# Kernel optimization log

Hardware: AMD Instinct MI355X
Metric: run time of the kernel (lower is better)

The kernel has to match this reference:

```python
import jax, jax.numpy as jnp
from jax import lax
import numpy as np
import math

# --- static config (matches init_kwargs) ---
B, L, C_IN = 64, 1024, 16
D, H, D_FF = 256, 8, 1024
HS, E_LAYERS, OUT = 256, 2, 1
MA, FACTOR = 25, 3
TOP_K = int(FACTOR * math.log(L))  # 20


def _ln(x, g, b, eps=1e-5):
    m = x.mean(-1, keepdims=True)
    v = ((x - m) ** 2).mean(-1, keepdims=True)
    return (x - m) / jnp.sqrt(v + eps) * g + b


def _series_decomp(x, k):
    # x: [B, L, C]; replicate-pad then moving average (AvgPool1d stride 1)
    pad = (k - 1) // 2
    front = jnp.repeat(x[:, :1, :], pad, axis=1)
    end = jnp.repeat(x[:, -1:, :], pad, axis=1)
    xp = jnp.concatenate([front, x, end], axis=1)  # [B, L+k-1, C]
    cs = jnp.cumsum(xp, axis=1)
    cs = jnp.concatenate([jnp.zeros_like(cs[:, :1]), cs], axis=1)
    mm = (cs[:, k:] - cs[:, :-k]) / k  # [B, L, C]
    return x - mm, mm


def _autocorrelation(q, k, v):
    # q,k,v: [B, L, H, E] -> eval-mode Autoformer AutoCorrelation
    Bq, Lq, Hq, Eq = q.shape
    qf = jnp.fft.rfft(q.transpose(0, 2, 3, 1), axis=-1)  # [B,H,E,F]
    kf = jnp.fft.rfft(k.transpose(0, 2, 3, 1), axis=-1)
    corr = jnp.fft.irfft(qf * jnp.conj(kf), n=Lq, axis=-1)  # [B,H,E,L]
    mean_value = corr.mean(axis=(1, 2))  # [B, L]
    weights, delay = lax.top_k(mean_value, TOP_K)  # [B, K]
    tmp_corr = jax.nn.softmax(weights, axis=-1)
    vals = v.transpose(0, 2, 3, 1)  # [B,H,E,L]
    init = jnp.arange(Lq)

    def step(acc, dw):
        d, w = dw  # d: [B] int, w: [B] float
        idx = (init[None, :] + d[:, None]) % Lq  # circular delayed gather == roll
        pat = jnp.take_along_axis(vals, idx[:, None, None, :], axis=-1)
        return acc + pat * w[:, None, None, None], None

    agg, _ = lax.scan(step, jnp.zeros_like(vals), (delay.T, tmp_corr.T))
    return agg.transpose(0, 3, 1, 2)  # [B, L, H, E]


def _forward(x_enc, conv1_w, conv1_b, conv2_w, conv2_b, cnn_ln_g, cnn_ln_b,
             proj_w, proj_b, proj_ln_g, proj_ln_b,
             Wq, bq, Wk, bk, Wv, bv, Wo, bo, Wff1, Wff2,
             rp1_w, rp1_b, rp_ln_g, rp_ln_b, rp2_w, rp2_b):
    Bb = x_enc.shape[0]
    dn = ('NCH', 'OIH', 'NCH')
    # CNN frontend (dropout = identity in eval)
    h = lax.conv_general_dilated(x_enc.transpose(0, 2, 1), conv1_w, (1,), [(1, 1)],
                                 dimension_numbers=dn) + conv1_b[None, :, None]
    h = jax.nn.relu(h)
    h = lax.conv_general_dilated(h, conv2_w, (1,), [(1, 1)],
                                 dimension_numbers=dn) + conv2_b[None, :, None]
    h = jax.nn.relu(h)
    enc = _ln(h.transpose(0, 2, 1), cnn_ln_g, cnn_ln_b)  # [B, L, D]

    pooled_parts = []
    for i in range(E_LAYERS):
        q = (enc @ Wq[i] + bq[i]).reshape(Bb, L, H, D // H)
        k = (enc @ Wk[i] + bk[i]).reshape(Bb, L, H, D // H)
        v = (enc @ Wv[i] + bv[i]).reshape(Bb, L, H, D // H)
        ac = _autocorrelation(q, k, v).reshape(Bb, L, D)
        new_x = ac @ Wo[i] + bo[i]
        x = enc + new_x
        x, _ = _series_decomp(x, MA)
        y = jax.nn.gelu(jnp.einsum('bld,fd->blf', x, Wff1[i]), approximate=False)
        y = jnp.einsum('blf,df->bld', y, Wff2[i])
        enc, _ = _series_decomp(x + y, MA)
        pooled_parts.append(enc[:, -1, :])

    pooled = jnp.concatenate(pooled_parts, axis=-1)  # [B, e_layers*D]
    input_embed = _ln(jax.nn.relu(x_enc.reshape(Bb, -1) @ proj_w + proj_b),
                      proj_ln_g, proj_ln_b)  # [B, HS]
    final = jnp.concatenate([pooled, input_embed], axis=-1)
    o = jax.nn.relu(final @ rp1_w + rp1_b)
    o = _ln(o, rp_ln_g, rp_ln_b)
    o = o @ rp2_w + rp2_b  # [B, 1]
    return o.squeeze(-1)


def setup_inputs() -> dict:
    key = jax.random.key(0)
    ks = iter(jax.random.split(key, 32))

    def nrm(shape, s=0.02):
        return jax.random.normal(next(ks), shape, jnp.float32) * s

    inp = {
        'x_enc': jax.random.normal(next(ks), (B, L, C_IN), jnp.float32),
        'conv1_w': nrm((D, C_IN, 3), 0.1), 'conv1_b': jnp.zeros((D,), jnp.float32),
        'conv2_w': nrm((D, D, 3), 0.05), 'conv2_b': jnp.zeros((D,), jnp.float32),
        'cnn_ln_g': jnp.ones((D,), jnp.float32), 'cnn_ln_b': jnp.zeros((D,), jnp.float32),
        'proj_w': nrm((L * C_IN, HS)), 'proj_b': jnp.zeros((HS,), jnp.float32),
        'proj_ln_g': jnp.ones((HS,), jnp.float32), 'proj_ln_b': jnp.zeros((HS,), jnp.float32),
        'Wq': nrm((E_LAYERS, D, D)), 'bq': jnp.zeros((E_LAYERS, D), jnp.float32),
        'Wk': nrm((E_LAYERS, D, D)), 'bk': jnp.zeros((E_LAYERS, D), jnp.float32),
        'Wv': nrm((E_LAYERS, D, D)), 'bv': jnp.zeros((E_LAYERS, D), jnp.float32),
        'Wo': nrm((E_LAYERS, D, D)), 'bo': jnp.zeros((E_LAYERS, D), jnp.float32),
        'Wff1': nrm((E_LAYERS, D_FF, D)),
        'Wff2': nrm((E_LAYERS, D, D_FF)),
        'rp1_w': nrm((E_LAYERS * D + HS, HS)), 'rp1_b': jnp.zeros((HS,), jnp.float32),
        'rp_ln_g': jnp.ones((HS,), jnp.float32), 'rp_ln_b': jnp.zeros((HS,), jnp.float32),
        'rp2_w': nrm((HS, OUT)), 'rp2_b': jnp.zeros((OUT,), jnp.float32),
    }
    return inp


def reference(x_enc, conv1_w, conv1_b, conv2_w, conv2_b, cnn_ln_g, cnn_ln_b,
              proj_w, proj_b, proj_ln_g, proj_ln_b,
              Wq, bq, Wk, bk, Wv, bv, Wo, bo, Wff1, Wff2,
              rp1_w, rp1_b, rp_ln_g, rp_ln_b, rp2_w, rp2_b):
    return _forward(x_enc, conv1_w, conv1_b, conv2_w, conv2_b, cnn_ln_g, cnn_ln_b,
                    proj_w, proj_b, proj_ln_g, proj_ln_b,
                    Wq, bq, Wk, bk, Wv, bv, Wo, bo, Wff1, Wff2,
                    rp1_w, rp1_b, rp_ln_g, rp_ln_b, rp2_w, rp2_b)
```

## Files before the change

kernel.cpp:

```cpp
#include <hip/hip_runtime.h>
#include <math.h>

#define FLAG_ACC     1
#define FLAG_RELU    2
#define FLAG_GELU    4
#define FLAG_ABF16   8
#define FLAG_OBF16  16
#define FLAG_RESB16 32

typedef __attribute__((ext_vector_type(8))) short short8;
typedef __attribute__((ext_vector_type(4))) short short4v;
typedef __attribute__((ext_vector_type(4))) float f32x4;

__device__ __forceinline__ short f2bf(float f) {
  unsigned u = __builtin_bit_cast(unsigned, f);
  unsigned r = u + 0x7fffu + ((u >> 16) & 1u);
  return (short)(r >> 16);
}
__device__ __forceinline__ float bf2f(short s) {
  unsigned u = ((unsigned)(unsigned short)s) << 16;
  return __builtin_bit_cast(float, u);
}
__device__ __forceinline__ void load_lds16(const void* g, void* lds) {
  __builtin_amdgcn_global_load_lds(
      (const __attribute__((address_space(1))) void*)g,
      (__attribute__((address_space(3))) void*)lds, 16, 0, 0);
}

__global__ __launch_bounds__(256) void gemm_f32(
    const float* __restrict__ A, const float* __restrict__ B, float* __restrict__ C,
    int M, int N, int K, int a_shift,
    const float* __restrict__ bias, const float* __restrict__ residual, int flags)
{
  __shared__ float As[16][65];
  __shared__ float Bs[16][64];
  const int tid = threadIdx.x;
  const int tx = tid & 15, ty = tid >> 4;
  const int row0 = blockIdx.y * 64;
  const int col0 = blockIdx.x * 64;
  int kbeg = 0, kend = K;
  if ((int)gridDim.z > 1) {
    int kchunk = ((K + (int)gridDim.z - 1) / (int)gridDim.z + 15) & ~15;
    kbeg = (int)blockIdx.z * kchunk;
    kend = min(K, kbeg + kchunk);
  }
  float acc[4][4] = {};
  const int a_m = tid >> 2;
  const int a_k = (tid & 3) << 2;
  const int b_n = (tid & 15) << 2;
  const int b_k = tid >> 4;
  for (int k0 = kbeg; k0 < kend; k0 += 16) {
    int srow = row0 + a_m + a_shift;
    float4 av = make_float4(0.f, 0.f, 0.f, 0.f);
    if (srow >= 0 && srow < M)
      av = *reinterpret_cast<const float4*>(A + (long long)srow * K + (k0 + a_k));
    As[a_k + 0][a_m] = av.x; As[a_k + 1][a_m] = av.y;
    As[a_k + 2][a_m] = av.z; As[a_k + 3][a_m] = av.w;
    float4 bv = make_float4(0.f, 0.f, 0.f, 0.f);
    int brow = k0 + b_k;
    if (brow < K)
      bv = *reinterpret_cast<const float4*>(B + (long long)brow * N + (col0 + b_n));
    Bs[b_k][b_n + 0] = bv.x; Bs[b_k][b_n + 1] = bv.y;
    Bs[b_k][b_n + 2] = bv.z; Bs[b_k][b_n + 3] = bv.w;
    __syncthreads();
#pragma unroll
    for (int kk = 0; kk < 16; kk++) {
      float ar[4], br[4];
#pragma unroll
      for (int i = 0; i < 4; i++) ar[i] = As[kk][ty * 4 + i];
#pragma unroll
      for (int j = 0; j < 4; j++) br[j] = Bs[kk][tx * 4 + j];
#pragma unroll
      for (int i = 0; i < 4; i++)
#pragma unroll
        for (int j = 0; j < 4; j++)
          acc[i][j] += ar[i] * br[j];
    }
    __syncthreads();
  }
  if ((int)gridDim.z > 1) {
#pragma unroll
    for (int i = 0; i < 4; i++) {
      int r = row0 + ty * 4 + i; if (r >= M) continue;
#pragma unroll
      for (int j = 0; j < 4; j++) {
        int c = col0 + tx * 4 + j; if (c >= N) continue;
        atomicAdd(&C[(long long)r * N + c], acc[i][j]);
      }
    }
    return;
  }
#pragma unroll
  for (int i = 0; i < 4; i++) {
    int r = row0 + ty * 4 + i; if (r >= M) continue;
#pragma unroll
    for (int j = 0; j < 4; j++) {
      int c = col0 + tx * 4 + j; if (c >= N) continue;
      float v = acc[i][j];
      if (bias)     v += bias[c];
      if (residual) v += residual[(long long)r * N + c];
      if (flags & FLAG_ACC)  v += C[(long long)r * N + c];
      if (flags & FLAG_RELU) v = fmaxf(v, 0.f);
      if (flags & FLAG_GELU) v = 0.5f * v * (1.f + erff(v * 0.70710678118654752f));
      C[(long long)r * N + c] = v;
    }
  }
}

__global__ __launch_bounds__(256) void gemm_bf16_bt(
    const void* __restrict__ Av, const short* __restrict__ Btb, void* __restrict__ Cv,
    const float* __restrict__ residual, const float* __restrict__ bias,
    int M, int N, int K, int lda, int flags, int tapped)
{
  __shared__ __align__(16) short Asl[8192];
  __shared__ __align__(16) short Bsl[8192];
  const int tid = threadIdx.x;
  const int row0 = blockIdx.x * 128;
  const int col0 = blockIdx.y * 128;
  const int lane = tid & 63;
  const int wave = tid >> 6;
  const int wm = (wave >> 1) * 64;
  const int wn = (wave & 1) * 64;
  const int fm = lane & 15;
  const int k8c = lane >> 4;
  const int mr = tid >> 1;
  const int mkc = (tid & 1) * 4;
  const int msw = mr & 7;
  const bool a_dma = (flags & FLAG_ABF16) && !tapped;

  f32x4 acc[4][4] = {};
  for (int k0 = 0; k0 < K; k0 += 64) {
    __syncthreads();
#pragma unroll
    for (int u = 0; u < 4; u++) {
      int p = (wave * 4 + u) * 64 + lane;
      int r = p >> 3;
      int kc = (p & 7) ^ (r & 7);
      load_lds16(Btb + (long long)(col0 + r) * K + k0 + kc * 8,
                 (char*)Bsl + (wave * 4 + u) * 1024);
    }
    if (a_dma) {
      const short* Ab = (const short*)Av;
#pragma unroll
      for (int u = 0; u < 4; u++) {
        int p = (wave * 4 + u) * 64 + lane;
        int r = p >> 3;
        int kc = (p & 7) ^ (r & 7);
        load_lds16(Ab + (long long)(row0 + r) * lda + k0 + kc * 8,
                   (char*)Asl + (wave * 4 + u) * 1024);
      }
    } else {
      int arow = row0 + mr + (tapped ? (k0 >> 8) - 1 : 0);
      int acol = tapped ? (k0 & 255) : k0;
      bool ok = (arow >= 0 && arow < M);
      if (flags & FLAG_ABF16) {
        const short* ga = (const short*)Av + (long long)arow * lda + acol + mkc * 8;
        short8 z;
#pragma unroll
        for (int u = 0; u < 8; u++) z[u] = 0;
#pragma unroll
        for (int j = 0; j < 4; j++) {
          short8 v = ok ? *(const short8*)(ga + j * 8) : z;
          *(short8*)&Asl[(mr * 8 + ((mkc + j) ^ msw)) * 8] = v;
        }
      } else {
        const float* ga = (const float*)Av + (long long)arow * lda + acol + mkc * 8;
#pragma unroll
        for (int j = 0; j < 4; j++) {
          float4 f0 = make_float4(0.f,0.f,0.f,0.f), f1 = f0;
          if (ok) { f0 = *(const float4*)(ga + j * 8); f1 = *(const float4*)(ga + j * 8 + 4); }
          short8 v;
          v[0]=f2bf(f0.x); v[1]=f2bf(f0.y); v[2]=f2bf(f0.z); v[3]=f2bf(f0.w);
          v[4]=f2bf(f1.x); v[5]=f2bf(f1.y); v[6]=f2bf(f1.z); v[7]=f2bf(f1.w);
          *(short8*)&Asl[(mr * 8 + ((mkc + j) ^ msw)) * 8] = v;
        }
      }
    }
    __syncthreads();
#pragma unroll
    for (int kk8 = 0; kk8 < 8; kk8 += 4) {
      short8 af[4], bf[4];
#pragma unroll
      for (int i = 0; i < 4; i++) {
        int r = wm + i * 16 + fm;
        af[i] = *(short8*)&Asl[(r * 8 + ((kk8 + k8c) ^ (r & 7))) * 8];
      }
#pragma unroll
      for (int j = 0; j < 4; j++) {
        int r = wn + j * 16 + fm;
        bf[j] = *(short8*)&Bsl[(r * 8 + ((kk8 + k8c) ^ (r & 7))) * 8];
      }
#pragma unroll
      for (int i = 0; i < 4; i++)
#pragma unroll
        for (int j = 0; j < 4; j++)
          acc[i][j] = __builtin_amdgcn_mfma_f32_16x16x32_bf16(af[i], bf[j], acc[i][j], 0, 0, 0);
    }
  }
#pragma unroll
  for (int i = 0; i < 4; i++) {
    const int mbase = row0 + wm + i * 16 + (lane >> 4) * 4;
#pragma unroll
    for (int j = 0; j < 4; j++) {
      const int n = col0 + wn + j * 16 + fm;
      const float bs = bias ? bias[n] : 0.f;
#pragma unroll
      for (int r = 0; r < 4; r++) {
        long long idx = (long long)(mbase + r) * N + n;
        float v = acc[i][j][r] + bs;
        if (residual) {
          if (flags & FLAG_RESB16) v += bf2f(((const short*)residual)[idx]);
          else                     v += residual[idx];
        }
        if (flags & FLAG_ACC)  v += ((const float*)Cv)[idx];
        if (flags & FLAG_RELU) v = fmaxf(v, 0.f);
        if (flags & FLAG_GELU) v = 0.5f * v * (1.f + erff(v * 0.70710678118654752f));
        if (flags & FLAG_OBF16) ((short*)Cv)[idx] = f2bf(v);
        else                    ((float*)Cv)[idx] = v;
      }
    }
  }
}

__global__ __launch_bounds__(256) void gemm_qkT(
    const short* __restrict__ Ab, const short* __restrict__ Bth,
    const short* __restrict__ Btl, float* __restrict__ QT,
    const float* __restrict__ bias, int K)
{
  __shared__ __align__(16) char smem[24576];
  short* Asl = (short*)smem;
  short* Bhi = (short*)(smem + 8192);
  short* Blo = (short*)(smem + 16384);
  const int tid = threadIdx.x;
  const int row0 = blockIdx.x * 128;
  const int col0 = blockIdx.y * 128;
  const int lane = tid & 63;
  const int wave = tid >> 6;
  const int wm = (wave >> 1) * 64;
  const int wn = (wave & 1) * 64;
  const int fm = lane & 15;
  const int k8c = lane >> 4;

  f32x4 acc[4][4] = {};
  for (int k0 = 0; k0 < K; k0 += 32) {
    __syncthreads();
#pragma unroll
    for (int u = 0; u < 2; u++) {
      int p = (wave + u * 4) * 64 + lane;
      int r = p >> 2;
      int kc = (p & 3) ^ ((r >> 1) & 3);
      long long ao = (long long)(row0 + r) * 256 + k0 + kc * 8;
      long long go = (long long)(col0 + r) * K + k0 + kc * 8;
      int lo = (wave + u * 4) * 1024;
      load_lds16(Ab + ao, (char*)Asl + lo);
      load_lds16(Bth + go, (char*)Bhi + lo);
      load_lds16(Btl + go, (char*)Blo + lo);
    }
    __syncthreads();
    short8 af[4], bh[4], bl[4];
#pragma unroll
    for (int i = 0; i < 4; i++) {
      int r = wm + i * 16 + fm;
      af[i] = *(short8*)&Asl[(r * 4 + (k8c ^ ((r >> 1) & 3))) * 8];
    }
#pragma unroll
    for (int j = 0; j < 4; j++) {
      int r = wn + j * 16 + fm;
      int p = (r * 4 + (k8c ^ ((r >> 1) & 3))) * 8;
      bh[j] = *(short8*)&Bhi[p];
      bl[j] = *(short8*)&Blo[p];
    }
#pragma unroll
    for (int i = 0; i < 4; i++)
#pragma unroll
      for (int j = 0; j < 4; j++) {
        acc[i][j] = __builtin_amdgcn_mfma_f32_16x16x32_bf16(af[i], bh[j], acc[i][j], 0, 0, 0);
        acc[i][j] = __builtin_amdgcn_mfma_f32_16x16x32_bf16(af[i], bl[j], acc[i][j], 0, 0, 0);
      }
  }
#pragma unroll
  for (int i = 0; i < 4; i++) {
    const int mbase = row0 + wm + i * 16 + (lane >> 4) * 4;
    const int bb = mbase >> 10;
    const int l  = mbase & 1023;
#pragma unroll
    for (int j = 0; j < 4; j++) {
      const int n = col0 + wn + j * 16 + fm;
      const float bs = bias[n];
      float4 o = make_float4(acc[i][j][0] + bs, acc[i][j][1] + bs,
                             acc[i][j][2] + bs, acc[i][j][3] + bs);
      *(float4*)&QT[((long long)(bb * 512 + n) << 10) + l] = o;
    }
  }
}

#define SKW(i) ((i) + ((i) >> 5))

__device__ __forceinline__ int rev4_10(int f) {
  return ((f & 3) << 8) | (((f >> 2) & 3) << 6) | (((f >> 4) & 3) << 4)
       | (((f >> 6) & 3) << 2) | ((f >> 8) & 3);
}

template<int M, bool INV>
__device__ __forceinline__ void fft_stage(const float2* __restrict__ s,
                                          float2* __restrict__ d,
                                          const float2* __restrict__ tw, int t) {
  constexpr int LOG2M = (M == 256) ? 8 : (M == 64) ? 6 : (M == 16) ? 4 : (M == 4) ? 2 : 0;
  const int j = t & (M - 1);
  const int base = ((t >> LOG2M) << (LOG2M + 2)) | j;
  float2 a = s[SKW(base)];
  float2 b = s[SKW(base + M)];
  float2 c = s[SKW(base + 2 * M)];
  float2 e = s[SKW(base + 3 * M)];
  float t0r = a.x + c.x, t0i = a.y + c.y;
  float t1r = a.x - c.x, t1i = a.y - c.y;
  float t2r = b.x + e.x, t2i = b.y + e.y;
  float t3r = b.x - e.x, t3i = b.y - e.y;
  float y0r = t0r + t2r, y0i = t0i + t2i;
  float y2r = t0r - t2r, y2i = t0i - t2i;
  float y1r, y1i, y3r, y3i;
  if (!INV) { y1r = t1r + t3i; y1i = t1i - t3r; y3r = t1r - t3i; y3i = t1i + t3r; }
  else      { y1r = t1r - t3i; y1i = t1i + t3r; y3r = t1r + t3i; y3i = t1i - t3r; }
  float2 w = tw[SKW(j << (8 - LOG2M))];
  float c1 = w.x, s1 = INV ? -w.y : w.y;
  float c2 = c1 * c1 - s1 * s1, s2 = 2.f * c1 * s1;
  float c3 = c2 * c1 - s2 * s1, s3 = c2 * s1 + s2 * c1;
  d[SKW(base)]         = make_float2(y0r, y0i);
  d[SKW(base + M)]     = make_float2(y1r * c1 - y1i * s1, y1r * s1 + y1i * c1);
  d[SKW(base + 2 * M)] = make_float2(y2r * c2 - y2i * s2, y2r * s2 + y2i * c2);
  d[SKW(base + 3 * M)] = make_float2(y3r * c3 - y3i * s3, y3r * s3 + y3i * c3);
}

__global__ __launch_bounds__(256) void fft_cross(
    const float* __restrict__ QT, float* __restrict__ Rpart)
{
  __shared__ float2 ping[1056], pong[1056], tw[264];
  const int tid = threadIdx.x;
  const int b = blockIdx.x & 63;
  const int g = blockIdx.x >> 6;
  {
    float s, c;
    sincosf(-1.5707963267948966f * (float)tid * (1.f / 256.f), &s, &c);
    tw[SKW(tid)] = make_float2(c, s);
  }
  const float* Qb = QT + (long long)b * 524288;
  const int c0 = g * 32;
  float4 qv = *(const float4*)(Qb + ((long long)c0 << 10) + tid * 4);
  float4 kv = *(const float4*)(Qb + ((long long)(256 + c0) << 10) + tid * 4);
  float aR[4] = {0.f, 0.f, 0.f, 0.f}, aI[4] = {0.f, 0.f, 0.f, 0.f};
  __syncthreads();
  for (int cc = 0; cc < 32; cc++) {
    const int i0 = tid * 4;
    ping[SKW(i0 + 0)] = make_float2(qv.x, kv.x);
    ping[SKW(i0 + 1)] = make_float2(qv.y, kv.y);
    ping[SKW(i0 + 2)] = make_float2(qv.z, kv.z);
    ping[SKW(i0 + 3)] = make_float2(qv.w, kv.w);
    if (cc < 31) {
      int c = c0 + cc + 1;
      qv = *(const float4*)(Qb + ((long long)c << 10) + tid * 4);
      kv = *(const float4*)(Qb + ((long long)(256 + c) << 10) + tid * 4);
    }
    __syncthreads();
    fft_stage<256, false>(ping, pong, tw, tid); __syncthreads();
    fft_stage<64,  false>(pong, ping, tw, tid); __syncthreads();
    fft_stage<16,  false>(ping, pong, tw, tid); __syncthreads();
    fft_stage<4,   false>(pong, ping, tw, tid); __syncthreads();
    fft_stage<1,   false>(ping, pong, tw, tid); __syncthreads();
#pragma unroll
    for (int u = 0; u < 4; u++) {
      int f = tid + (u << 8);
      float2 z1 = pong[SKW(rev4_10(f))];
      float2 z2 = pong[SKW(rev4_10((1024 - f) & 1023))];
      float Qr = 0.5f * (z1.x + z2.x), Qi = 0.5f * (z1.y - z2.y);
      float Kr = 0.5f * (z1.y + z2.y), Ki = 0.5f * (z2.x - z1.x);
      aR[u] += Qr * Kr + Qi * Ki;
      aI[u] += Qi * Kr - Qr * Ki;
    }
  }
  float* Rp = Rpart + (long long)(g * 64 + b) * 2048;
#pragma unroll
  for (int u = 0; u < 4; u++) {
    Rp[tid + (u << 8)] = aR[u];
    Rp[1024 + tid + (u << 8)] = aI[u];
  }
}

__global__ __launch_bounds__(256) void fft_inv(
    const float* __restrict__ Rpart, float* __restrict__ MV)
{
  __shared__ float2 ping[1056], pong[1056], tw[264];
  const int tid = threadIdx.x;
  const int b = blockIdx.x;
  {
    float s, c;
    sincosf(-1.5707963267948966f * (float)tid * (1.f / 256.f), &s, &c);
    tw[SKW(tid)] = make_float2(c, s);
  }
#pragma unroll
  for (int u = 0; u < 4; u++) {
    int f = tid + (u << 8);
    float sr = 0.f, si = 0.f;
#pragma unroll
    for (int g = 0; g < 8; g++) {
      const float* Rp = Rpart + (long long)(g * 64 + b) * 2048;
      sr += Rp[f];
      si += Rp[1024 + f];
    }
    ping[SKW(f)] = make_float2(sr, si);
  }
  __syncthreads();
  fft_stage<256, true>(ping, pong, tw, tid); __syncthreads();
  fft_stage<64,  true>(pong, ping, tw, tid); __syncthreads();
  fft_stage<16,  true>(ping, pong, tw, tid); __syncthreads();
  fft_stage<4,   true>(pong, ping, tw, tid); __syncthreads();
  fft_stage<1,   true>(ping, pong, tw, tid); __syncthreads();
  const float sc = 1.f / (1024.f * 256.f);
#pragma unroll
  for (int u = 0; u < 4; u++) {
    int p = tid + (u << 8);
    MV[(long long)b * 1024 + rev4_10(p)] = pong[SKW(p)].x * sc;
  }
}

__global__ void prep_weights(
    const float* __restrict__ conv2_w, const float* __restrict__ Wq,
    const float* __restrict__ Wk, const float* __restrict__ Wff1,
    const float* __restrict__ Wff2,
    const float* __restrict__ bq, const float* __restrict__ bk,
    short* __restrict__ CB2Tb, short* __restrict__ QKTH, short* __restrict__ QKTL,
    short* __restrict__ WFF1b, short* __restrict__ WFF2b, float* __restrict__ BQK)
{
  const int total = 196608 + 262144 + 524288 + 524288 + 1024;
  for (int idx = blockIdx.x * 256 + threadIdx.x; idx < total;
       idx += gridDim.x * 256) {
    int t = idx;
    if (t < 196608) {
      int o = t / 768, rem = t % 768, kk = rem >> 8, i = rem & 255;
      CB2Tb[t] = f2bf(conv2_w[(o * 256 + i) * 3 + kk]);
    } else if ((t -= 196608) < 262144) {
      int L = t >> 17, rem = t & 131071, r = rem >> 8, k = rem & 255;
      float val = (r < 256) ? Wq[L * 65536 + k * 256 + r]
                            : Wk[L * 65536 + k * 256 + (r - 256)];
      short h = f2bf(val);
      QKTH[t] = h;
      QKTL[t] = f2bf(val - bf2f(h));
    } else if ((t -= 262144) < 524288) {
      WFF1b[t] = f2bf(Wff1[t]);
    } else if ((t -= 524288) < 524288) {
      WFF2b[t] = f2bf(Wff2[t]);
    } else {
      t -= 524288;
      int L = t >> 9, j = t & 511;
      BQK[t] = (j < 256) ? bq[L * 256 + j] : bk[L * 256 + (j - 256)];
    }
  }
}

__global__ void vo_finish(const float* __restrict__ WVO, const float* __restrict__ Wo,
                          const float* __restrict__ bv, const float* __restrict__ bo,
                          short* __restrict__ WVOTb, float* __restrict__ BVO)
{
  const int total = 131072 + 512;
  for (int idx = blockIdx.x * 256 + threadIdx.x; idx < total;
       idx += gridDim.x * 256) {
    if (idx < 131072) {
      int L = idx >> 16, rem = idx & 65535, n = rem >> 8, k = rem & 255;
      WVOTb[idx] = f2bf(WVO[L * 65536 + k * 256 + n]);
    } else {
      int j = idx - 131072;
      int L = j >> 8, n = j & 255;
      float acc = bo[L * 256 + n];
      for (int k = 0; k < 256; k++)
        acc += bv[L * 256 + k] * Wo[(long long)L * 65536 + k * 256 + n];
      BVO[j] = acc;
    }
  }
}

__global__ __launch_bounds__(256) void conv1_direct(
    const float* __restrict__ x, const float* __restrict__ w,
    const float* __restrict__ bias, short* __restrict__ out)
{
  __shared__ float xs[66][16];
  const int b = blockIdx.y, lg = blockIdx.x, tid = threadIdx.x;
  const int l0 = lg * 64;
  for (int idx = tid; idx < 1056; idx += 256) {
    int r = idx >> 4, c = idx & 15;
    int l = l0 + r - 1;
    xs[r][c] = (l >= 0 && l < 1024) ? x[((long long)b * 1024 + l) * 16 + c] : 0.f;
  }
  float wr[48];
#pragma unroll
  for (int u = 0; u < 48; u++) wr[u] = w[tid * 48 + u];
  const float bs = bias[tid];
  __syncthreads();
  for (int r = 0; r < 64; r++) {
    float acc = bs;
#pragma unroll
    for (int i = 0; i < 16; i++) {
      acc += xs[r + 0][i] * wr[i * 3 + 0];
      acc += xs[r + 1][i] * wr[i * 3 + 1];
      acc += xs[r + 2][i] * wr[i * 3 + 2];
    }
    out[((long long)b * 1024 + l0 + r) * 256 + tid] = f2bf(fmaxf(acc, 0.f));
  }
}

__global__ void fixup_conv_b(short* __restrict__ h, const short* __restrict__ src,
                             const float* __restrict__ w, const float* __restrict__ bias)
{
  int b = blockIdx.x >> 1;
  int l = (blockIdx.x & 1) ? 1023 : 0;
  int o = threadIdx.x;
  float acc = bias[o];
  for (int kk = 0; kk < 3; kk++) {
    int t = l + kk - 1;
    if (t < 0 || t > 1023) continue;
    const short* srow = src + ((long long)b * 1024 + t) * 256;
    const float* wrow = w + (long long)o * 256 * 3 + kk;
    for (int i = 0; i < 256; i++) acc += bf2f(srow[i]) * wrow[(long long)i * 3];
  }
  h[((long long)b * 1024 + l) * 256 + o] = f2bf(fmaxf(acc, 0.f));
}

__global__ __launch_bounds__(256) void ln_rows4(
    const float* __restrict__ in, float* __restrict__ out,
    const float* __restrict__ g, const float* __restrict__ b,
    int prerelu, int out_stride, int out_off)
{
  const int row = blockIdx.x * 4 + (threadIdx.x >> 6);
  const int lane = threadIdx.x & 63;
  float4 x = ((const float4*)(in + (long long)row * 256))[lane];
  if (prerelu) {
    x.x = fmaxf(x.x, 0.f); x.y = fmaxf(x.y, 0.f);
    x.z = fmaxf(x.z, 0.f); x.w = fmaxf(x.w, 0.f);
  }
  float s = x.x + x.y + x.z + x.w;
#pragma unroll
  for (int o = 32; o > 0; o >>= 1) s += __shfl_xor(s, o, 64);
  float mean = s * (1.f / 256.f);
  float4 d = make_float4(x.x - mean, x.y - mean, x.z - mean, x.w - mean);
  float s2 = d.x * d.x + d.y * d.y + d.z * d.z + d.w * d.w;
#pragma unroll
  for (int o = 32; o > 0; o >>= 1) s2 += __shfl_xor(s2, o, 64);
  float rsd = rsqrtf(s2 * (1.f / 256.f) + 1e-5f);
  float4 gg = ((const float4*)g)[lane];
  float4 bb = ((const float4*)b)[lane];
  float4 o4 = make_float4(d.x * rsd * gg.x + bb.x, d.y * rsd * gg.y + bb.y,
                          d.z * rsd * gg.z + bb.z, d.w * rsd * gg.w + bb.w);
  ((float4*)(out + (long long)row * out_stride + out_off))[lane] = o4;
}

__global__ __launch_bounds__(256) void ln_rows4bb(
    const short* __restrict__ in, short* __restrict__ out,
    const float* __restrict__ g, const float* __restrict__ b)
{
  const int row = blockIdx.x * 4 + (threadIdx.x >> 6);
  const int lane = threadIdx.x & 63;
  short4v xb = ((const short4v*)in)[(long long)row * 64 + lane];
  float4 x = make_float4(bf2f(xb[0]), bf2f(xb[1]), bf2f(xb[2]), bf2f(xb[3]));
  float s = x.x + x.y + x.z + x.w;
#pragma unroll
  for (int o = 32; o > 0; o >>= 1) s += __shfl_xor(s, o, 64);
  float mean = s * (1.f / 256.f);
  float4 d = make_float4(x.x - mean, x.y - mean, x.z - mean, x.w - mean);
  float s2 = d.x * d.x + d.y * d.y + d.z * d.z + d.w * d.w;
#pragma unroll
  for (int o = 32; o > 0; o >>= 1) s2 += __shfl_xor(s2, o, 64);
  float rsd = rsqrtf(s2 * (1.f / 256.f) + 1e-5f);
  float4 gg = ((const float4*)g)[lane];
  float4 bb = ((const float4*)b)[lane];
  short4v o4;
  o4[0] = f2bf(d.x * rsd * gg.x + bb.x);
  o4[1] = f2bf(d.y * rsd * gg.y + bb.y);
  o4[2] = f2bf(d.z * rsd * gg.z + bb.z);
  o4[3] = f2bf(d.w * rsd * gg.w + bb.w);
  ((short4v*)out)[(long long)row * 64 + lane] = o4;
}

__global__ void decomp4bf(const short* __restrict__ in, short* __restrict__ out,
                          float* __restrict__ fin, int finoff)
{
  const int id = blockIdx.x;
  const int c = id & 7;
  const int s = id >> 3;
  const int b = c + 8 * (s >> 8);
  const int lg = s & 255;
  const int l = lg * 4 + (threadIdx.x >> 6);
  const int c4 = threadIdx.x & 63;
  const short4v* base = (const short4v*)(in + (long long)b * 262144);
  float4 acc = make_float4(0.f, 0.f, 0.f, 0.f);
#pragma unroll
  for (int j = -12; j <= 12; j++) {
    int t = l + j;
    t = t < 0 ? 0 : (t > 1023 ? 1023 : t);
    short4v x = base[t * 64 + c4];
    acc.x += bf2f(x[0]); acc.y += bf2f(x[1]);
    acc.z += bf2f(x[2]); acc.w += bf2f(x[3]);
  }
  short4v x0 = base[l * 64 + c4];
  float4 o = make_float4(bf2f(x0[0]) - acc.x * (1.f / 25.f),
                         bf2f(x0[1]) - acc.y * (1.f / 25.f),
                         bf2f(x0[2]) - acc.z * (1.f / 25.f),
                         bf2f(x0[3]) - acc.w * (1.f / 25.f));
  short4v ob;
  ob[0] = f2bf(o.x); ob[1] = f2bf(o.y); ob[2] = f2bf(o.z); ob[3] = f2bf(o.w);
  ((short4v*)out)[((long long)b * 1024 + l) * 64 + c4] = ob;
  if (l == 1023) {
    float* f = fin + (long long)b * 768 + finoff + c4 * 4;
    f[0] = o.x; f[1] = o.y; f[2] = o.z; f[3] = o.w;
  }
}

__global__ void decomp4b(const short* __restrict__ in, short* __restrict__ out)
{
  const int id = blockIdx.x;
  const int c = id & 7;
  const int s = id >> 3;
  const int b = c + 8 * (s >> 8);
  const int lg = s & 255;
  const int l = lg * 4 + (threadIdx.x >> 6);
  const int c4 = threadIdx.x & 63;
  const short4v* base = (const short4v*)(in + (long long)b * 262144);
  float4 acc = make_float4(0.f, 0.f, 0.f, 0.f);
#pragma unroll
  for (int j = -12; j <= 12; j++) {
    int t = l + j;
    t = t < 0 ? 0 : (t > 1023 ? 1023 : t);
    short4v x = base[t * 64 + c4];
    acc.x += bf2f(x[0]); acc.y += bf2f(x[1]);
    acc.z += bf2f(x[2]); acc.w += bf2f(x[3]);
  }
  short4v x0 = base[l * 64 + c4];
  short4v o;
  o[0] = f2bf(bf2f(x0[0]) - acc.x * (1.f / 25.f));
  o[1] = f2bf(bf2f(x0[1]) - acc.y * (1.f / 25.f));
  o[2] = f2bf(bf2f(x0[2]) - acc.z * (1.f / 25.f));
  o[3] = f2bf(bf2f(x0[3]) - acc.w * (1.f / 25.f));
  ((short4v*)(out + (long long)b * 262144))[l * 64 + c4] = o;
}

__global__ __launch_bounds__(64) void topk_softmax_wave(
    const float* __restrict__ mv, float* __restrict__ wts, int* __restrict__ dly)
{
  const int b = blockIdx.x, lane = threadIdx.x;
  float v[16];
#pragma unroll
  for (int j = 0; j < 16; j++)
    v[j] = mv[(long long)b * 1024 + lane + 64 * j];
  float selv = 0.f; int seli = 0;
  for (int it = 0; it < 20; it++) {
    float bv = -1e30f; int bi = 0x7fffffff;
#pragma unroll
    for (int j = 0; j < 16; j++) {
      float x = v[j]; int idx = lane + 64 * j;
      if (x > bv || (x == bv && idx < bi)) { bv = x; bi = idx; }
    }
#pragma unroll
    for (int off = 32; off > 0; off >>= 1) {
      float ov = __shfl_xor(bv, off, 64);
      int   oi = __shfl_xor(bi, off, 64);
      if (ov > bv || (ov == bv && oi < bi)) { bv = ov; bi = oi; }
    }
    if (lane == it) { selv = bv; seli = bi; }
    if ((bi & 63) == lane) v[bi >> 6] = -1e30f;
  }
  const float w0 = __shfl(selv, 0, 64);
  float e = (lane < 20) ? __expf(selv - w0) : 0.f;
  float s = e;
#pragma unroll
  for (int off = 32; off > 0; off >>= 1) s += __shfl_xor(s, off, 64);
  if (lane < 20) {
    wts[b * 20 + lane] = e / s;
    dly[b * 20 + lane] = seli;
  }
}

__global__ void agg4b(const short* __restrict__ enc, const float* __restrict__ wts,
                      const int* __restrict__ dly, short* __restrict__ out)
{
  const int id = blockIdx.x;
  const int c = id & 7;
  const int s = id >> 3;
  const int b = c + 8 * (s >> 8);
  const int lg = s & 255;
  const int l = lg * 4 + (threadIdx.x >> 6);
  const int c4 = threadIdx.x & 63;
  const short4v* vb = (const short4v*)(enc + (long long)b * 262144);
  float4 acc = make_float4(0.f, 0.f, 0.f, 0.f);
  for (int kk = 0; kk < 20; kk++) {
    int d = dly[b * 20 + kk];
    float w = wts[b * 20 + kk];
    short4v x = vb[((l + d) & 1023) * 64 + c4];
    acc.x += w * bf2f(x[0]); acc.y += w * bf2f(x[1]);
    acc.z += w * bf2f(x[2]); acc.w += w * bf2f(x[3]);
  }
  short4v o;
  o[0] = f2bf(acc.x); o[1] = f2bf(acc.y); o[2] = f2bf(acc.z); o[3] = f2bf(acc.w);
  ((short4v*)(out + (long long)b * 262144))[l * 64 + c4] = o;
}

__global__ void init_bias(float* __restrict__ C, const float* __restrict__ bias)
{
  C[(long long)blockIdx.x * 256 + threadIdx.x] = bias[threadIdx.x];
}

__global__ void rp2_kernel(const float* __restrict__ x, const float* __restrict__ w,
                           const float* __restrict__ bias, float* __restrict__ out)
{
  __shared__ float red[4];
  int b = blockIdx.x, tid = threadIdx.x;
  float p = x[b * 256 + tid] * w[tid];
#pragma unroll
  for (int o = 32; o > 0; o >>= 1) p += __shfl_down(p, o, 64);
  if ((tid & 63) == 0) red[tid >> 6] = p;
  __syncthreads();
  if (tid == 0) out[b] = red[0] + red[1] + red[2] + red[3] + bias[0];
}

static inline void gemm(hipStream_t s, const float* A, const float* B, float* C,
                        int M, int N, int K, int shift, const float* bias,
                        const float* res, int flags, int splitz = 1)
{
  dim3 g((N + 63) / 64, (M + 63) / 64, splitz);
  gemm_f32<<<g, dim3(256), 0, s>>>(A, B, C, M, N, K, shift, bias, res, flags);
}

extern "C" void kernel_launch(void* const* d_in, const int* in_sizes, int n_in,
                              void* d_out, int out_size, void* d_ws, size_t ws_size,
                              hipStream_t stream)
{
  const float* x_enc  = (const float*)d_in[0];
  const float* conv1_w= (const float*)d_in[1];
  const float* conv1_b= (const float*)d_in[2];
  const float* conv2_w= (const float*)d_in[3];
  const float* conv2_b= (const float*)d_in[4];
  const float* cnn_g  = (const float*)d_in[5];
  const float* cnn_b  = (const float*)d_in[6];
  const float* proj_w = (const float*)d_in[7];
  const float* proj_b = (const float*)d_in[8];
  const float* pln_g  = (const float*)d_in[9];
  const float* pln_b  = (const float*)d_in[10];
  const float* Wq     = (const float*)d_in[11];
  const float* bq     = (const float*)d_in[12];
  const float* Wk     = (const float*)d_in[13];
  const float* bk     = (const float*)d_in[14];
  const float* Wv     = (const float*)d_in[15];
  const float* bv     = (const float*)d_in[16];
  const float* Wo     = (const float*)d_in[17];
  const float* bo     = (const float*)d_in[18];
  const float* Wff1   = (const float*)d_in[19];
  const float* Wff2   = (const float*)d_in[20];
  const float* rp1_w  = (const float*)d_in[21];
  const float* rp1_b  = (const float*)d_in[22];
  const float* rln_g  = (const float*)d_in[23];
  const float* rln_b  = (const float*)d_in[24];
  const float* rp2_w  = (const float*)d_in[25];
  const float* rp2_b  = (const float*)d_in[26];
  (void)in_sizes; (void)n_in;

  const size_t BLD = 64ull * 1024 * 256;
  size_t need;
  {
    size_t o = 3 * BLD
             + 98304 + 131072 + 131072 + 262144 + 262144
             + 65536 + 512 + 1024
             + 1048576 + 1280 + 1280 + 16384 + 49152 + 16384 + 16384;
    need = o * sizeof(float);
  }
  if (ws_size < need) {
    hipMemsetAsync(d_out, 0, (size_t)out_size * sizeof(float), stream);
    return;
  }

  float* ws = (float*)d_ws;
  size_t off = 0;
  auto alloc = [&](size_t n) { float* p = ws + off; off += n; return p; };
  float* BUF0 = alloc(BLD);
  float* BUF1 = alloc(BLD);
  float* BUF2 = alloc(BLD);
  short* CB2Tb = (short*)alloc(98304);
  short* QKTH  = (short*)alloc(131072);
  short* QKTL  = (short*)alloc(131072);
  short* WFF1b = (short*)alloc(262144);
  short* WFF2b = (short*)alloc(262144);
  short* WVOTb = (short*)alloc(65536);
  float* BVO  = alloc(512);
  float* BQK  = alloc(1024);
  float* MV16 = alloc(1048576);
  float* WTS  = alloc(1280);
  int*   DLY  = (int*)alloc(1280);
  float* PE   = alloc(16384);
  float* FIN  = alloc(49152);
  float* O1   = alloc(16384);
  float* O2   = alloc(16384);
  float* WVO  = BUF0;
  short* ENC  = (short*)BUF2;
  float* QT   = BUF0;
  float* MV   = BUF2 + 8388608;

  const int M = 65536;
  dim3 blk(256);

  prep_weights<<<1024, blk, 0, stream>>>(conv2_w, Wq, Wk, Wff1, Wff2, bq, bk,
                                         CB2Tb, QKTH, QKTL, WFF1b, WFF2b, BQK);
  for (int i = 0; i < 2; i++)
    gemm(stream, Wv + (size_t)i * 65536, Wo + (size_t)i * 65536,
         WVO + (size_t)i * 65536, 256, 256, 256, 0, nullptr, nullptr, 0);
  vo_finish<<<516, blk, 0, stream>>>(WVO, Wo, bv, bo, WVOTb, BVO);

  conv1_direct<<<dim3(16, 64), blk, 0, stream>>>(x_enc, conv1_w, conv1_b, (short*)BUF0);
  gemm_bf16_bt<<<dim3(512, 2), blk, 0, stream>>>(
      BUF0, CB2Tb, BUF1, nullptr, conv2_b, M, 256, 768, 256,
      FLAG_ABF16 | FLAG_RELU | FLAG_OBF16, 1);
  fixup_conv_b<<<128, blk, 0, stream>>>((short*)BUF1, (const short*)BUF0,
                                        conv2_w, conv2_b);
  ln_rows4bb<<<16384, blk, 0, stream>>>((const short*)BUF1, ENC, cnn_g, cnn_b);

  for (int i = 0; i < 2; i++) {
    gemm_qkT<<<dim3(512, 4), blk, 0, stream>>>(
        ENC, QKTH + (size_t)i * 131072, QKTL + (size_t)i * 131072,
        QT, BQK + i * 512, 256);
    fft_cross<<<512, blk, 0, stream>>>(QT, MV16);
    fft_inv<<<64, blk, 0, stream>>>(MV16, MV);
    topk_softmax_wave<<<64, dim3(64), 0, stream>>>(MV, WTS, DLY);
    agg4b<<<dim3(16384), blk, 0, stream>>>(ENC, WTS, DLY, (short*)BUF0);
    gemm_bf16_bt<<<dim3(512, 2), blk, 0, stream>>>(
        BUF0, WVOTb + (size_t)i * 65536, BUF1, (const float*)ENC, BVO + i * 256,
        M, 256, 256, 256, FLAG_ABF16 | FLAG_OBF16 | FLAG_RESB16, 0);
    decomp4b<<<16384, blk, 0, stream>>>((const short*)BUF1, (short*)BUF0);
    for (int c = 0; c < 2; c++) {
      const short* xd = (const short*)BUF0 + (size_t)c * 32768 * 256;
      gemm_bf16_bt<<<dim3(256, 8), blk, 0, stream>>>(
          xd, WFF1b + (size_t)i * 262144, BUF2, nullptr, nullptr,
          32768, 1024, 256, 256, FLAG_ABF16 | FLAG_GELU | FLAG_OBF16, 0);
      gemm_bf16_bt<<<dim3(256, 2), blk, 0, stream>>>(
          BUF2, WFF2b + (size_t)i * 262144,
          (short*)BUF1 + (size_t)c * 32768 * 256,
          (const float*)xd, nullptr,
          32768, 256, 1024, 1024, FLAG_ABF16 | FLAG_RESB16 | FLAG_OBF16, 0);
    }
    decomp4bf<<<16384, blk, 0, stream>>>((const short*)BUF1, ENC, FIN, i * 256);
  }

  init_bias<<<64, blk, 0, stream>>>(PE, proj_b);
  gemm(stream, x_enc, proj_w, PE, 64, 256, 16384, 0, nullptr, nullptr, 0, 32);
  ln_rows4<<<16, blk, 0, stream>>>(PE, FIN, pln_g, pln_b, 1, 768, 512);
  init_bias<<<64, blk, 0, stream>>>(O1, rp1_b);
  gemm(stream, FIN, rp1_w, O1, 64, 256, 768, 0, nullptr, nullptr, 0, 4);
  ln_rows4<<<16, blk, 0, stream>>>(O1, O2, rln_g, rln_b, 1, 256, 0);
  rp2_kernel<<<64, blk, 0, stream>>>(O2, rp2_w, rp2_b, (float*)d_out);
}
```

Baseline: 1.494 ms.

## Batch four channel FFTs per block in place and double the fft_cross grid

The FFT stage is rewritten to run in place and to process four channel pairs per thread per stage, so the twiddle load and barriers are amortized across four transforms. fft_cross now launches 1024 blocks of 16 channels each instead of 512 blocks of 32, which gives more parallelism. fft_inv reduces 16 partial spectra instead of 8, and the partial and MV buffers are reassigned. The cost is about 34KB of LDS per block for the four buffers, which may lower occupancy, plus more partial-sum traffic in fft_inv.

```diff
diff --git a/kernel.cpp b/kernel.cpp
--- a/kernel.cpp
+++ b/kernel.cpp
@@ -301,40 +301,44 @@
        | (((f >> 6) & 3) << 2) | ((f >> 8) & 3);
 }
 
-template<int M, bool INV>
-__device__ __forceinline__ void fft_stage(const float2* __restrict__ s,
-                                          float2* __restrict__ d,
-                                          const float2* __restrict__ tw, int t) {
+template<int M, bool INV, int NCH>
+__device__ __forceinline__ void fft_stageN(float2 (*__restrict__ buf)[1056],
+                                           const float2* __restrict__ tw, int t) {
   constexpr int LOG2M = (M == 256) ? 8 : (M == 64) ? 6 : (M == 16) ? 4 : (M == 4) ? 2 : 0;
   const int j = t & (M - 1);
   const int base = ((t >> LOG2M) << (LOG2M + 2)) | j;
-  float2 a = s[SKW(base)];
-  float2 b = s[SKW(base + M)];
-  float2 c = s[SKW(base + 2 * M)];
-  float2 e = s[SKW(base + 3 * M)];
-  float t0r = a.x + c.x, t0i = a.y + c.y;
-  float t1r = a.x - c.x, t1i = a.y - c.y;
-  float t2r = b.x + e.x, t2i = b.y + e.y;
-  float t3r = b.x - e.x, t3i = b.y - e.y;
-  float y0r = t0r + t2r, y0i = t0i + t2i;
-  float y2r = t0r - t2r, y2i = t0i - t2i;
-  float y1r, y1i, y3r, y3i;
-  if (!INV) { y1r = t1r + t3i; y1i = t1i - t3r; y3r = t1r - t3i; y3i = t1i + t3r; }
-  else      { y1r = t1r - t3i; y1i = t1i + t3r; y3r = t1r + t3i; y3i = t1i - t3r; }
   float2 w = tw[SKW(j << (8 - LOG2M))];
-  float c1 = w.x, s1 = INV ? -w.y : w.y;
-  float c2 = c1 * c1 - s1 * s1, s2 = 2.f * c1 * s1;
-  float c3 = c2 * c1 - s2 * s1, s3 = c2 * s1 + s2 * c1;
-  d[SKW(base)]         = make_float2(y0r, y0i);
-  d[SKW(base + M)]     = make_float2(y1r * c1 - y1i * s1, y1r * s1 + y1i * c1);
-  d[SKW(base + 2 * M)] = make_float2(y2r * c2 - y2i * s2, y2r * s2 + y2i * c2);
-  d[SKW(base + 3 * M)] = make_float2(y3r * c3 - y3i * s3, y3r * s3 + y3i * c3);
+  const float c1 = w.x, s1 = INV ? -w.y : w.y;
+  const float c2 = c1 * c1 - s1 * s1, s2 = 2.f * c1 * s1;
+  const float c3 = c2 * c1 - s2 * s1, s3 = c2 * s1 + s2 * c1;
+#pragma unroll
+  for (int ch = 0; ch < NCH; ch++) {
+    float2* s = buf[ch];
+    float2 a0 = s[SKW(base)];
+    float2 b0 = s[SKW(base + M)];
+    float2 d0 = s[SKW(base + 2 * M)];
+    float2 e0 = s[SKW(base + 3 * M)];
+    float t0r = a0.x + d0.x, t0i = a0.y + d0.y;
+    float t1r = a0.x - d0.x, t1i = a0.y - d0.y;
+    float t2r = b0.x + e0.x, t2i = b0.y + e0.y;
+    float t3r = b0.x - e0.x, t3i = b0.y - e0.y;
+    float y0r = t0r + t2r, y0i = t0i + t2i;
+    float y2r = t0r - t2r, y2i = t0i - t2i;
+    float y1r, y1i, y3r, y3i;
+    if (!INV) { y1r = t1r + t3i; y1i = t1i - t3r; y3r = t1r - t3i; y3i = t1i + t3r; }
+    else      { y1r = t1r - t3i; y1i = t1i + t3r; y3r = t1r + t3i; y3i = t1i - t3r; }
+    s[SKW(base)]         = make_float2(y0r, y0i);
+    s[SKW(base + M)]     = make_float2(y1r * c1 - y1i * s1, y1r * s1 + y1i * c1);
+    s[SKW(base + 2 * M)] = make_float2(y2r * c2 - y2i * s2, y2r * s2 + y2i * c2);
+    s[SKW(base + 3 * M)] = make_float2(y3r * c3 - y3i * s3, y3r * s3 + y3i * c3);
+  }
 }
 
 __global__ __launch_bounds__(256) void fft_cross(
     const float* __restrict__ QT, float* __restrict__ Rpart)
 {
-  __shared__ float2 ping[1056], pong[1056], tw[264];
+  __shared__ float2 buf[4][1056];
+  __shared__ float2 tw[264];
   const int tid = threadIdx.x;
   const int b = blockIdx.x & 63;
   const int g = blockIdx.x >> 6;
@@ -344,38 +348,54 @@
     tw[SKW(tid)] = make_float2(c, s);
   }
   const float* Qb = QT + (long long)b * 524288;
-  const int c0 = g * 32;
-  float4 qv = *(const float4*)(Qb + ((long long)c0 << 10) + tid * 4);
-  float4 kv = *(const float4*)(Qb + ((long long)(256 + c0) << 10) + tid * 4);
+  const int c0 = g * 16;
+  float4 qv[4], kv[4];
+#pragma unroll
+  for (int c = 0; c < 4; c++) {
+    qv[c] = *(const float4*)(Qb + ((long long)(c0 + c) << 10) + tid * 4);
+    kv[c] = *(const float4*)(Qb + ((long long)(256 + c0 + c) << 10) + tid * 4);
+  }
   float aR[4] = {0.f, 0.f, 0.f, 0.f}, aI[4] = {0.f, 0.f, 0.f, 0.f};
   __syncthreads();
-  for (int cc = 0; cc < 32; cc++) {
+  for (int q4 = 0; q4 < 4; q4++) {
     const int i0 = tid * 4;
-    ping[SKW(i0 + 0)] = make_float2(qv.x, kv.x);
-    ping[SKW(i0 + 1)] = make_float2(qv.y, kv.y);
-    ping[SKW(i0 + 2)] = make_float2(qv.z, kv.z);
-    ping[SKW(i0 + 3)] = make_float2(qv.w, kv.w);
-    if (cc < 31) {
-      int c = c0 + cc + 1;
-      qv = *(const float4*)(Qb + ((long long)c << 10) + tid * 4);
-      kv = *(const float4*)(Qb + ((long long)(256 + c) << 10) + tid * 4);
+#pragma unroll
+    for (int c = 0; c < 4; c++) {
+      buf[c][SKW(i0 + 0)] = make_float2(qv[c].x, kv[c].x);
+      buf[c][SKW(i0 + 1)] = make_float2(qv[c].y, kv[c].y);
+      buf[c][SKW(i0 + 2)] = make_float2(qv[c].z, kv[c].z);
+      buf[c][SKW(i0 + 3)] = make_float2(qv[c].w, kv[c].w);
+    }
+    if (q4 < 3) {
+      const int cb = c0 + (q4 + 1) * 4;
+#pragma unroll
+      for (int c = 0; c < 4; c++) {
+        qv[c] = *(const float4*)(Qb + ((long long)(cb + c) << 10) + tid * 4);
+        kv[c] = *(const float4*)(Qb + ((long long)(256 + cb + c) << 10) + tid * 4);
+      }
     }
     __syncthreads();
-    fft_stage<256, false>(ping, pong, tw, tid); __syncthreads();
-    fft_stage<64,  false>(pong, ping, tw, tid); __syncthreads();
-    fft_stage<16,  false>(ping, pong, tw, tid); __syncthreads();
-    fft_stage<4,   false>(pong, ping, tw, tid); __syncthreads();
-    fft_stage<1,   false>(ping, pong, tw, tid); __syncthreads();
+    fft_stageN<256, false, 4>(buf, tw, tid); __syncthreads();
+    fft_stageN<64,  false, 4>(buf, tw, tid); __syncthreads();
+    fft_stageN<16,  false, 4>(buf, tw, tid); __syncthreads();
+    fft_stageN<4,   false, 4>(buf, tw, tid); __syncthreads();
+    fft_stageN<1,   false, 4>(buf, tw, tid); __syncthreads();
 #pragma unroll
     for (int u = 0; u < 4; u++) {
-      int f = tid + (u << 8);
-      float2 z1 = pong[SKW(rev4_10(f))];
-      float2 z2 = pong[SKW(rev4_10((1024 - f) & 1023))];
-      float Qr = 0.5f * (z1.x + z2.x), Qi = 0.5f * (z1.y - z2.y);
-      float Kr = 0.5f * (z1.y + z2.y), Ki = 0.5f * (z2.x - z1.x);
-      aR[u] += Qr * Kr + Qi * Ki;
-      aI[u] += Qi * Kr - Qr * Ki;
-    }
+      const int f = tid + (u << 8);
+      const int p1 = SKW(rev4_10(f));
+      const int p2 = SKW(rev4_10((1024 - f) & 1023));
+#pragma unroll
+      for (int c = 0; c < 4; c++) {
+        float2 z1 = buf[c][p1];
+        float2 z2 = buf[c][p2];
+        float Qr = 0.5f * (z1.x + z2.x), Qi = 0.5f * (z1.y - z2.y);
+        float Kr = 0.5f * (z1.y + z2.y), Ki = 0.5f * (z2.x - z1.x);
+        aR[u] += Qr * Kr + Qi * Ki;
+        aI[u] += Qi * Kr - Qr * Ki;
+      }
+    }
+    __syncthreads();
   }
   float* Rp = Rpart + (long long)(g * 64 + b) * 2048;
 #pragma unroll
@@ -388,7 +408,7 @@
 __global__ __launch_bounds__(256) void fft_inv(
     const float* __restrict__ Rpart, float* __restrict__ MV)
 {
-  __shared__ float2 ping[1056], pong[1056], tw[264];
+  __shared__ float2 ping[1056], tw[264];
   const int tid = threadIdx.x;
   const int b = blockIdx.x;
   {
@@ -401,7 +421,7 @@
     int f = tid + (u << 8);
     float sr = 0.f, si = 0.f;
 #pragma unroll
-    for (int g = 0; g < 8; g++) {
+    for (int g = 0; g < 16; g++) {
       const float* Rp = Rpart + (long long)(g * 64 + b) * 2048;
       sr += Rp[f];
       si += Rp[1024 + f];
@@ -409,16 +429,17 @@
     ping[SKW(f)] = make_float2(sr, si);
   }
   __syncthreads();
-  fft_stage<256, true>(ping, pong, tw, tid); __syncthreads();
-  fft_stage<64,  true>(pong, ping, tw, tid); __syncthreads();
-  fft_stage<16,  true>(ping, pong, tw, tid); __syncthreads();
-  fft_stage<4,   true>(pong, ping, tw, tid); __syncthreads();
-  fft_stage<1,   true>(ping, pong, tw, tid); __syncthreads();
+  float2 (*bp)[1056] = reinterpret_cast<float2 (*)[1056]>(ping);
+  fft_stageN<256, true, 1>(bp, tw, tid); __syncthreads();
+  fft_stageN<64,  true, 1>(bp, tw, tid); __syncthreads();
+  fft_stageN<16,  true, 1>(bp, tw, tid); __syncthreads();
+  fft_stageN<4,   true, 1>(bp, tw, tid); __syncthreads();
+  fft_stageN<1,   true, 1>(bp, tw, tid); __syncthreads();
   const float sc = 1.f / (1024.f * 256.f);
 #pragma unroll
   for (int u = 0; u < 4; u++) {
     int p = tid + (u << 8);
-    MV[(long long)b * 1024 + rev4_10(p)] = pong[SKW(p)].x * sc;
+    MV[(long long)b * 1024 + rev4_10(p)] = ping[SKW(p)].x * sc;
   }
 }
 
@@ -797,7 +818,8 @@
   float* WVO  = BUF0;
   short* ENC  = (short*)BUF2;
   float* QT   = BUF0;
-  float* MV   = BUF2 + 8388608;
+  float* RP   = BUF2 + 8388608;
+  float* MV   = MV16;
 
   const int M = 65536;
   dim3 blk(256);
@@ -821,8 +843,8 @@
     gemm_qkT<<<dim3(512, 4), blk, 0, stream>>>(
         ENC, QKTH + (size_t)i * 131072, QKTL + (size_t)i * 131072,
         QT, BQK + i * 512, 256);
-    fft_cross<<<512, blk, 0, stream>>>(QT, MV16);
-    fft_inv<<<64, blk, 0, stream>>>(MV16, MV);
+    fft_cross<<<dim3(1024), blk, 0, stream>>>(QT, RP);
+    fft_inv<<<64, blk, 0, stream>>>(RP, MV);
     topk_softmax_wave<<<64, dim3(64), 0, stream>>>(MV, WTS, DLY);
     agg4b<<<dim3(16384), blk, 0, stream>>>(ENC, WTS, DLY, (short*)BUF0);
     gemm_bf16_bt<<<dim3(512, 2), blk, 0, stream>>>(
```

Result: no change. 1.493 ms (-0.1%).
